# Kernel tuning notes

Measured on AMD Instinct MI355X. Metric: run time of the kernel, lower is better.

## Reference

```python
import jax, jax.numpy as jnp
import numpy as np

N_NODES = 40000
N_EDGES = 640000
D_IN = 128
D_OUT = 128


def setup_inputs() -> dict:
    key = jax.random.key(0)
    k_feat, k_src, k_dst, k_ws, k_wn = jax.random.split(key, 5)
    feat = jax.random.normal(k_feat, (N_NODES, D_IN), dtype=jnp.float32)
    src = jax.random.randint(k_src, (N_EDGES,), 0, N_NODES, dtype=jnp.int32)
    dst = jax.random.randint(k_dst, (N_EDGES,), 0, N_NODES, dtype=jnp.int32)
    # Glorot-ish init for the two dense layers
    scale = 1.0 / np.sqrt(D_IN)
    W_self = jax.random.normal(k_ws, (D_IN, D_OUT), dtype=jnp.float32) * scale
    W_neigh = jax.random.normal(k_wn, (D_IN, D_OUT), dtype=jnp.float32) * scale
    b_self = jnp.zeros((D_OUT,), dtype=jnp.float32)
    b_neigh = jnp.zeros((D_OUT,), dtype=jnp.float32)
    return {"feat": feat, "src": src, "dst": dst,
            "W_self": W_self, "b_self": b_self,
            "W_neigh": W_neigh, "b_neigh": b_neigh}


def reference(feat, src, dst, W_self, b_self, W_neigh, b_neigh):
    # --- mean aggregation: copy_src('h','m') + mean('m','neigh') ---
    # Gather source features along edges, segment-sum into dst, divide by in-degree.
    msgs = feat[src]  # [E, D_in]
    neigh_sum = jax.ops.segment_sum(msgs, dst, num_segments=N_NODES)  # [N, D_in]
    deg = jax.ops.segment_sum(jnp.ones((src.shape[0],), feat.dtype), dst,
                              num_segments=N_NODES)  # [N]
    # DGL mean reducer yields 0 for nodes with no incoming edges.
    h_neigh = neigh_sum / jnp.maximum(deg, 1.0)[:, None]
    # --- fc_self(h_self) + fc_neigh(h_neigh) ---
    rst = (feat @ W_self + b_self) + (h_neigh @ W_neigh + b_neigh)
    return rst
```

## Files before the change

kernel.cpp:

```cpp
#include <hip/hip_runtime.h>
#include <cstddef>

constexpr int NN  = 40000;
constexpr int NE  = 640000;
constexpr int DIM = 128;
constexpr int CAP = 48;
constexpr int PLANE = NN * 64;

typedef __attribute__((ext_vector_type(8))) short short8;
typedef __attribute__((ext_vector_type(4))) float floatx4;

__device__ __forceinline__ unsigned short f2bf(float x) {
    union { float f; unsigned int i; } v; v.f = x;
    unsigned int u = v.i;
    return (unsigned short)((u + 0x7fffu + ((u >> 16) & 1u)) >> 16);
}
__device__ __forceinline__ float bflo2f(unsigned int u) {
    union { unsigned int i; float f; } v; v.i = u << 16; return v.f;
}
__device__ __forceinline__ float bfhi2f(unsigned int u) {
    union { unsigned int i; float f; } v; v.i = u & 0xffff0000u; return v.f;
}

__global__ __launch_bounds__(256) void k_prep(
    const float* __restrict__ feat, const float* __restrict__ Wself,
    const float* __restrict__ Wneigh, unsigned short* __restrict__ featb,
    unsigned short* __restrict__ Wc, int* __restrict__ cnt)
{
    int b = blockIdx.x, t = threadIdx.x;
    if (b < 2500) {
        int idx8 = b * 256 + t;
        int n  = idx8 >> 4;
        int d0 = (idx8 & 15) << 3;
        const float4* fp =
            reinterpret_cast<const float4*>(feat + (size_t)n * DIM + d0);
        float4 v0 = fp[0], v1 = fp[1];
        unsigned int p0 = (unsigned int)f2bf(v0.x) | ((unsigned int)f2bf(v0.y) << 16);
        unsigned int p1 = (unsigned int)f2bf(v0.z) | ((unsigned int)f2bf(v0.w) << 16);
        unsigned int p2 = (unsigned int)f2bf(v1.x) | ((unsigned int)f2bf(v1.y) << 16);
        unsigned int p3 = (unsigned int)f2bf(v1.z) | ((unsigned int)f2bf(v1.w) << 16);
        int plane = d0 >> 6, off = d0 & 63;
        *reinterpret_cast<uint4*>(
            featb + (size_t)plane * PLANE + (size_t)n * 64 + off) =
            make_uint4(p0, p1, p2, p3);
    } else if (b < 2628) {
        int idx = (b - 2500) * 256 + t;
        int c = idx >> 13, n = (idx >> 6) & 127, kp = idx & 63;
        int k = c * 64 + kp;
        float w = (k < DIM) ? Wself[(size_t)k * DIM + n]
                            : Wneigh[(size_t)(k - DIM) * DIM + n];
        Wc[idx] = f2bf(w);
    } else {
        int i = (b - 2628) * 256 + t;
        if (i < NN) cnt[i] = 0;
    }
}

__global__ __launch_bounds__(256) void k_fill(
    const int* __restrict__ src, const int* __restrict__ dst,
    int* __restrict__ cnt, unsigned short* __restrict__ colf)
{
    int e = blockIdx.x * blockDim.x + threadIdx.x;
    if (e < NE) {
        int d = dst[e];
        int pos = atomicAdd(&cnt[d], 1);
        if (pos < CAP) colf[d * CAP + pos] = (unsigned short)src[e];
    }
}

__global__ __launch_bounds__(256) void k_gather(
    const unsigned int* __restrict__ fb32,
    const int* __restrict__ cnt,
    const unsigned short* __restrict__ colf,
    unsigned int* __restrict__ hnb32)
{
    int gtid = blockIdx.x * blockDim.x + threadIdx.x;
    int n = gtid >> 6;
    if (n >= NN) return;
    int lane = threadIdx.x & 63;

    int deg = cnt[n];
    int m = min(deg, CAP);
    int sv = (lane < m) ? (int)colf[n * CAP + lane] : 0;

    int vb = (lane >> 5) * (NN * 32) + (lane & 31);
    float ax0 = 0.f, ay0 = 0.f, ax1 = 0.f, ay1 = 0.f;
    int i = 0;
    for (; i + 3 < m; i += 4) {
        int s0 = __shfl(sv, i),     s1 = __shfl(sv, i + 1);
        int s2 = __shfl(sv, i + 2), s3 = __shfl(sv, i + 3);
        unsigned int u0 = fb32[vb + s0 * 32];
        unsigned int u1 = fb32[vb + s1 * 32];
        unsigned int u2 = fb32[vb + s2 * 32];
        unsigned int u3 = fb32[vb + s3 * 32];
        ax0 += bflo2f(u0); ay0 += bfhi2f(u0);
        ax1 += bflo2f(u1); ay1 += bfhi2f(u1);
        ax0 += bflo2f(u2); ay0 += bfhi2f(u2);
        ax1 += bflo2f(u3); ay1 += bfhi2f(u3);
    }
    for (; i < m; ++i) {
        int s0 = __shfl(sv, i);
        unsigned int u0 = fb32[vb + s0 * 32];
        ax0 += bflo2f(u0); ay0 += bfhi2f(u0);
    }
    float inv = 1.0f / fmaxf((float)deg, 1.0f);
    float ax = (ax0 + ax1) * inv, ay = (ay0 + ay1) * inv;
    hnb32[vb + n * 32] = (unsigned int)f2bf(ax) | ((unsigned int)f2bf(ay) << 16);
}

__global__ __launch_bounds__(320) void k_gemm(
    const unsigned short* __restrict__ featb,
    const unsigned short* __restrict__ hnb,
    const unsigned short* __restrict__ Wc,
    const float* __restrict__ bself, const float* __restrict__ bneigh,
    float* __restrict__ out)
{
    __shared__ unsigned short As[160 * 64];
    __shared__ unsigned short Bs[128 * 64];

    int t = threadIdx.x;
    int w = t >> 6;
    int lane = t & 63;
    int base_m = blockIdx.x * 160;

    floatx4 acc[2][8];
    #pragma unroll
    for (int a = 0; a < 2; ++a)
        #pragma unroll
        for (int b = 0; b < 8; ++b) acc[a][b] = (floatx4)0.f;

    for (int c = 0; c < 4; ++c) {
        const unsigned short* srcp =
            ((c < 2) ? featb + (size_t)c * PLANE
                     : hnb + (size_t)(c - 2) * PLANE) + (size_t)base_m * 64;
        #pragma unroll
        for (int it = 0; it < 4; ++it) {
            int slot = t + it * 320;
            __builtin_amdgcn_global_load_lds(
                (const __attribute__((address_space(1))) unsigned int*)(srcp + slot * 8),
                (__attribute__((address_space(3))) unsigned int*)(As + slot * 8),
                16, 0, 0);
        }
        if (t < 256) {
            const unsigned short* bp = Wc + (size_t)c * 128 * 64;
            #pragma unroll
            for (int it = 0; it < 4; ++it) {
                int slot = t + it * 256;
                __builtin_amdgcn_global_load_lds(
                    (const __attribute__((address_space(1))) unsigned int*)(bp + slot * 8),
                    (__attribute__((address_space(3))) unsigned int*)(Bs + slot * 8),
                    16, 0, 0);
            }
        }
        __syncthreads();

        #pragma unroll
        for (int s = 0; s < 2; ++s) {
            int koff = s * 32 + (lane >> 4) * 8;
            short8 af[2];
            #pragma unroll
            for (int mt = 0; mt < 2; ++mt) {
                int m = w * 32 + mt * 16 + (lane & 15);
                af[mt] = *reinterpret_cast<const short8*>(As + m * 64 + koff);
            }
            #pragma unroll
            for (int nt = 0; nt < 8; ++nt) {
                int n = nt * 16 + (lane & 15);
                short8 bf = *reinterpret_cast<const short8*>(Bs + n * 64 + koff);
                acc[0][nt] = __builtin_amdgcn_mfma_f32_16x16x32_bf16(
                    af[0], bf, acc[0][nt], 0, 0, 0);
                acc[1][nt] = __builtin_amdgcn_mfma_f32_16x16x32_bf16(
                    af[1], bf, acc[1][nt], 0, 0, 0);
            }
        }
        __syncthreads();
    }

    int colb = lane & 15;
    int quad = lane >> 4;
    #pragma unroll
    for (int nt = 0; nt < 8; ++nt) {
        int col = nt * 16 + colb;
        float bb = bself[col] + bneigh[col];
        #pragma unroll
        for (int mt = 0; mt < 2; ++mt) {
            #pragma unroll
            for (int r = 0; r < 4; ++r) {
                int row = base_m + w * 32 + mt * 16 + quad * 4 + r;
                out[(size_t)row * DIM + col] = acc[mt][nt][r] + bb;
            }
        }
    }
}

extern "C" void kernel_launch(void* const* d_in, const int* in_sizes, int n_in,
                              void* d_out, int out_size, void* d_ws, size_t ws_size,
                              hipStream_t stream)
{
    const float* feat   = (const float*)d_in[0];
    const int*   src    = (const int*)d_in[1];
    const int*   dst    = (const int*)d_in[2];
    const float* Wself  = (const float*)d_in[3];
    const float* bself  = (const float*)d_in[4];
    const float* Wneigh = (const float*)d_in[5];
    const float* bneigh = (const float*)d_in[6];
    float* out = (float*)d_out;

    char* ws = (char*)d_ws;
    unsigned short* featb = (unsigned short*)(ws);
    unsigned short* hnb   = (unsigned short*)(ws + 10240000);
    unsigned short* colf  = (unsigned short*)(ws + 20480000);
    unsigned short* Wc    = (unsigned short*)(ws + 24320000);
    int*            cnt   = (int*)(ws + 24385536);

    k_prep<<<2785, 256, 0, stream>>>(feat, Wself, Wneigh, featb, Wc, cnt);

    k_fill<<<(NE + 255) / 256, 256, 0, stream>>>(src, dst, cnt, colf);

    k_gather<<<(NN * 64) / 256, 256, 0, stream>>>(
        (const unsigned int*)featb, cnt, colf, (unsigned int*)hnb);

    k_gemm<<<NN / 160, 320, 0, stream>>>(featb, hnb, Wc, bself, bneigh, out);
}
```

Before: 148.7 us.

## Fuse neighbor gather into GEMM kernel, writing mean aggregates directly to LDS

New measurement: 210.0 us. +41.2%, slower.

```diff
diff --git a/kernel.cpp b/kernel.cpp
--- a/kernel.cpp
+++ b/kernel.cpp
@@ -68,49 +68,11 @@
     }
 }
 
-__global__ __launch_bounds__(256) void k_gather(
+__global__ __launch_bounds__(320) void k_gg(
+    const unsigned short* __restrict__ featb,
     const unsigned int* __restrict__ fb32,
     const int* __restrict__ cnt,
     const unsigned short* __restrict__ colf,
-    unsigned int* __restrict__ hnb32)
-{
-    int gtid = blockIdx.x * blockDim.x + threadIdx.x;
-    int n = gtid >> 6;
-    if (n >= NN) return;
-    int lane = threadIdx.x & 63;
-
-    int deg = cnt[n];
-    int m = min(deg, CAP);
-    int sv = (lane < m) ? (int)colf[n * CAP + lane] : 0;
-
-    int vb = (lane >> 5) * (NN * 32) + (lane & 31);
-    float ax0 = 0.f, ay0 = 0.f, ax1 = 0.f, ay1 = 0.f;
-    int i = 0;
-    for (; i + 3 < m; i += 4) {
-        int s0 = __shfl(sv, i),     s1 = __shfl(sv, i + 1);
-        int s2 = __shfl(sv, i + 2), s3 = __shfl(sv, i + 3);
-        unsigned int u0 = fb32[vb + s0 * 32];
-        unsigned int u1 = fb32[vb + s1 * 32];
-        unsigned int u2 = fb32[vb + s2 * 32];
-        unsigned int u3 = fb32[vb + s3 * 32];
-        ax0 += bflo2f(u0); ay0 += bfhi2f(u0);
-        ax1 += bflo2f(u1); ay1 += bfhi2f(u1);
-        ax0 += bflo2f(u2); ay0 += bfhi2f(u2);
-        ax1 += bflo2f(u3); ay1 += bfhi2f(u3);
-    }
-    for (; i < m; ++i) {
-        int s0 = __shfl(sv, i);
-        unsigned int u0 = fb32[vb + s0 * 32];
-        ax0 += bflo2f(u0); ay0 += bfhi2f(u0);
-    }
-    float inv = 1.0f / fmaxf((float)deg, 1.0f);
-    float ax = (ax0 + ax1) * inv, ay = (ay0 + ay1) * inv;
-    hnb32[vb + n * 32] = (unsigned int)f2bf(ax) | ((unsigned int)f2bf(ay) << 16);
-}
-
-__global__ __launch_bounds__(320) void k_gemm(
-    const unsigned short* __restrict__ featb,
-    const unsigned short* __restrict__ hnb,
     const unsigned short* __restrict__ Wc,
     const float* __restrict__ bself, const float* __restrict__ bneigh,
     float* __restrict__ out)
@@ -129,18 +91,11 @@
         #pragma unroll
         for (int b = 0; b < 8; ++b) acc[a][b] = (floatx4)0.f;
 
+    unsigned int* As32 = reinterpret_cast<unsigned int*>(As);
+    int j = lane >> 5;
+    int u = lane & 31;
+
     for (int c = 0; c < 4; ++c) {
-        const unsigned short* srcp =
-            ((c < 2) ? featb + (size_t)c * PLANE
-                     : hnb + (size_t)(c - 2) * PLANE) + (size_t)base_m * 64;
-        #pragma unroll
-        for (int it = 0; it < 4; ++it) {
-            int slot = t + it * 320;
-            __builtin_amdgcn_global_load_lds(
-                (const __attribute__((address_space(1))) unsigned int*)(srcp + slot * 8),
-                (__attribute__((address_space(3))) unsigned int*)(As + slot * 8),
-                16, 0, 0);
-        }
         if (t < 256) {
             const unsigned short* bp = Wc + (size_t)c * 128 * 64;
             #pragma unroll
@@ -150,6 +105,82 @@
                     (const __attribute__((address_space(1))) unsigned int*)(bp + slot * 8),
                     (__attribute__((address_space(3))) unsigned int*)(Bs + slot * 8),
                     16, 0, 0);
+            }
+        }
+
+        if (c < 2) {
+            const unsigned short* srcp =
+                featb + (size_t)c * PLANE + (size_t)base_m * 64;
+            #pragma unroll
+            for (int it = 0; it < 4; ++it) {
+                int slot = t + it * 320;
+                __builtin_amdgcn_global_load_lds(
+                    (const __attribute__((address_space(1))) unsigned int*)(srcp + slot * 8),
+                    (__attribute__((address_space(3))) unsigned int*)(As + slot * 8),
+                    16, 0, 0);
+            }
+        } else {
+            const unsigned int* pb = fb32 + (size_t)(c - 2) * (NN * 32);
+            for (int kk = 0; kk < 32; kk += 2) {
+                int ln0 = w * 32 + kk, ln1 = ln0 + 1;
+                int n0 = base_m + ln0, n1 = base_m + ln1;
+                int deg0 = cnt[n0], deg1 = cnt[n1];
+                int m0 = min(deg0, CAP), m1 = min(deg1, CAP);
+                int sv0 = (lane < m0) ? (int)colf[n0 * CAP + lane] : 0;
+                int sv1 = (lane < m1) ? (int)colf[n1 * CAP + lane] : 0;
+                float ax0 = 0.f, ay0 = 0.f, ax1 = 0.f, ay1 = 0.f;
+                {
+                    unsigned int va[8], vb_[8];
+                    int ia[8], ib[8];
+                    #pragma unroll
+                    for (int q = 0; q < 8; ++q) {
+                        ia[q] = 2 * q + j;
+                        ib[q] = 2 * q + j;
+                        int sa = __shfl(sv0, ia[q]);
+                        int sb = __shfl(sv1, ib[q]);
+                        va[q]  = pb[sa * 32 + u];
+                        vb_[q] = pb[sb * 32 + u];
+                    }
+                    #pragma unroll
+                    for (int q = 0; q < 8; ++q) {
+                        if (ia[q] < m0) { ax0 += bflo2f(va[q]);  ay0 += bfhi2f(va[q]); }
+                        if (ib[q] < m1) { ax1 += bflo2f(vb_[q]); ay1 += bfhi2f(vb_[q]); }
+                    }
+                }
+                for (int i = 16; i < m0; i += 16) {
+                    unsigned int va[8]; int ia[8];
+                    #pragma unroll
+                    for (int q = 0; q < 8; ++q) {
+                        ia[q] = i + 2 * q + j;
+                        int sa = __shfl(sv0, ia[q] < CAP ? ia[q] : 0);
+                        va[q] = pb[sa * 32 + u];
+                    }
+                    #pragma unroll
+                    for (int q = 0; q < 8; ++q)
+                        if (ia[q] < m0) { ax0 += bflo2f(va[q]); ay0 += bfhi2f(va[q]); }
+                }
+                for (int i = 16; i < m1; i += 16) {
+                    unsigned int vb2[8]; int ib[8];
+                    #pragma unroll
+                    for (int q = 0; q < 8; ++q) {
+                        ib[q] = i + 2 * q + j;
+                        int sb = __shfl(sv1, ib[q] < CAP ? ib[q] : 0);
+                        vb2[q] = pb[sb * 32 + u];
+                    }
+                    #pragma unroll
+                    for (int q = 0; q < 8; ++q)
+                        if (ib[q] < m1) { ax1 += bflo2f(vb2[q]); ay1 += bfhi2f(vb2[q]); }
+                }
+                ax0 += __shfl_xor(ax0, 32); ay0 += __shfl_xor(ay0, 32);
+                ax1 += __shfl_xor(ax1, 32); ay1 += __shfl_xor(ay1, 32);
+                if (lane < 32) {
+                    float inv0 = 1.0f / fmaxf((float)deg0, 1.0f);
+                    float inv1 = 1.0f / fmaxf((float)deg1, 1.0f);
+                    As32[ln0 * 32 + u] = (unsigned int)f2bf(ax0 * inv0)
+                                       | ((unsigned int)f2bf(ay0 * inv0) << 16);
+                    As32[ln1 * 32 + u] = (unsigned int)f2bf(ax1 * inv1)
+                                       | ((unsigned int)f2bf(ay1 * inv1) << 16);
+                }
             }
         }
         __syncthreads();
@@ -208,17 +239,14 @@
 
     char* ws = (char*)d_ws;
     unsigned short* featb = (unsigned short*)(ws);
-    unsigned short* hnb   = (unsigned short*)(ws + 10240000);
-    unsigned short* colf  = (unsigned short*)(ws + 20480000);
-    unsigned short* Wc    = (unsigned short*)(ws + 24320000);
-    int*            cnt   = (int*)(ws + 24385536);
+    unsigned short* colf  = (unsigned short*)(ws + 10240000);
+    unsigned short* Wc    = (unsigned short*)(ws + 14080000);
+    int*            cnt   = (int*)(ws + 14145536);
 
     k_prep<<<2785, 256, 0, stream>>>(feat, Wself, Wneigh, featb, Wc, cnt);
 
     k_fill<<<(NE + 255) / 256, 256, 0, stream>>>(src, dst, cnt, colf);
 
-    k_gather<<<(NN * 64) / 256, 256, 0, stream>>>(
-        (const unsigned int*)featb, cnt, colf, (unsigned int*)hnb);
-
-    k_gemm<<<NN / 160, 320, 0, stream>>>(featb, hnb, Wc, bself, bneigh, out);
-}
+    k_gg<<<NN / 160, 320, 0, stream>>>(
+        featb, (const unsigned int*)featb, cnt, colf, Wc, bself, bneigh, out);
+}
```

## Split gather into quarter-column planes and XOR-swizzle GEMM LDS tiles

Applied to the files above, without the earlier changes.

Result: slower. 165.8 us (+11.5%).

```diff
diff --git a/kernel.cpp b/kernel.cpp
--- a/kernel.cpp
+++ b/kernel.cpp
@@ -6,6 +6,7 @@
 constexpr int DIM = 128;
 constexpr int CAP = 48;
 constexpr int PLANE = NN * 64;
+constexpr int PL4   = NN * 32;
 
 typedef __attribute__((ext_vector_type(8))) short short8;
 typedef __attribute__((ext_vector_type(4))) float floatx4;
@@ -24,8 +25,9 @@
 
 __global__ __launch_bounds__(256) void k_prep(
     const float* __restrict__ feat, const float* __restrict__ Wself,
-    const float* __restrict__ Wneigh, unsigned short* __restrict__ featb,
-    unsigned short* __restrict__ Wc, int* __restrict__ cnt)
+    const float* __restrict__ Wneigh, unsigned short* __restrict__ featb2,
+    unsigned short* __restrict__ featb4, unsigned short* __restrict__ Wc,
+    int* __restrict__ cnt)
 {
     int b = blockIdx.x, t = threadIdx.x;
     if (b < 2500) {
@@ -39,10 +41,11 @@
         unsigned int p1 = (unsigned int)f2bf(v0.z) | ((unsigned int)f2bf(v0.w) << 16);
         unsigned int p2 = (unsigned int)f2bf(v1.x) | ((unsigned int)f2bf(v1.y) << 16);
         unsigned int p3 = (unsigned int)f2bf(v1.z) | ((unsigned int)f2bf(v1.w) << 16);
-        int plane = d0 >> 6, off = d0 & 63;
+        uint4 pk = make_uint4(p0, p1, p2, p3);
         *reinterpret_cast<uint4*>(
-            featb + (size_t)plane * PLANE + (size_t)n * 64 + off) =
-            make_uint4(p0, p1, p2, p3);
+            featb2 + (size_t)(d0 >> 6) * PLANE + (size_t)n * 64 + (d0 & 63)) = pk;
+        *reinterpret_cast<uint4*>(
+            featb4 + (size_t)(d0 >> 5) * PL4 + (size_t)n * 32 + (d0 & 31)) = pk;
     } else if (b < 2628) {
         int idx = (b - 2500) * 256 + t;
         int c = idx >> 13, n = (idx >> 6) & 127, kp = idx & 63;
@@ -69,43 +72,47 @@
 }
 
 __global__ __launch_bounds__(256) void k_gather(
-    const unsigned int* __restrict__ fb32,
+    const unsigned int* __restrict__ fb4,
     const int* __restrict__ cnt,
     const unsigned short* __restrict__ colf,
     unsigned int* __restrict__ hnb32)
 {
-    int gtid = blockIdx.x * blockDim.x + threadIdx.x;
-    int n = gtid >> 6;
-    if (n >= NN) return;
+    int b = blockIdx.x;
+    int c = b & 3;
+    int n = ((b >> 2) << 2) + (threadIdx.x >> 6);
     int lane = threadIdx.x & 63;
+    int j = lane >> 4;
+    int u = lane & 15;
 
     int deg = cnt[n];
     int m = min(deg, CAP);
     int sv = (lane < m) ? (int)colf[n * CAP + lane] : 0;
 
-    int vb = (lane >> 5) * (NN * 32) + (lane & 31);
-    float ax0 = 0.f, ay0 = 0.f, ax1 = 0.f, ay1 = 0.f;
-    int i = 0;
-    for (; i + 3 < m; i += 4) {
-        int s0 = __shfl(sv, i),     s1 = __shfl(sv, i + 1);
-        int s2 = __shfl(sv, i + 2), s3 = __shfl(sv, i + 3);
-        unsigned int u0 = fb32[vb + s0 * 32];
-        unsigned int u1 = fb32[vb + s1 * 32];
-        unsigned int u2 = fb32[vb + s2 * 32];
-        unsigned int u3 = fb32[vb + s3 * 32];
-        ax0 += bflo2f(u0); ay0 += bfhi2f(u0);
-        ax1 += bflo2f(u1); ay1 += bfhi2f(u1);
-        ax0 += bflo2f(u2); ay0 += bfhi2f(u2);
-        ax1 += bflo2f(u3); ay1 += bfhi2f(u3);
-    }
-    for (; i < m; ++i) {
-        int s0 = __shfl(sv, i);
-        unsigned int u0 = fb32[vb + s0 * 32];
-        ax0 += bflo2f(u0); ay0 += bfhi2f(u0);
-    }
-    float inv = 1.0f / fmaxf((float)deg, 1.0f);
-    float ax = (ax0 + ax1) * inv, ay = (ay0 + ay1) * inv;
-    hnb32[vb + n * 32] = (unsigned int)f2bf(ax) | ((unsigned int)f2bf(ay) << 16);
+    const unsigned int* pb = fb4 + (size_t)c * (NN * 16);
+    float ax = 0.f, ay = 0.f;
+    for (int i = 0; i < m; i += 16) {
+        int i0 = i + j, i1 = i + 4 + j, i2 = i + 8 + j, i3 = i + 12 + j;
+        int s0 = __shfl(sv, i0), s1 = __shfl(sv, i1);
+        int s2 = __shfl(sv, i2), s3 = __shfl(sv, i3);
+        unsigned int v0 = pb[s0 * 16 + u];
+        unsigned int v1 = pb[s1 * 16 + u];
+        unsigned int v2 = pb[s2 * 16 + u];
+        unsigned int v3 = pb[s3 * 16 + u];
+        if (i0 < m) { ax += bflo2f(v0); ay += bfhi2f(v0); }
+        if (i1 < m) { ax += bflo2f(v1); ay += bfhi2f(v1); }
+        if (i2 < m) { ax += bflo2f(v2); ay += bfhi2f(v2); }
+        if (i3 < m) { ax += bflo2f(v3); ay += bfhi2f(v3); }
+    }
+    ax += __shfl_xor(ax, 16); ay += __shfl_xor(ay, 16);
+    ax += __shfl_xor(ax, 32); ay += __shfl_xor(ay, 32);
+    if (lane < 16) {
+        float inv = 1.0f / fmaxf((float)deg, 1.0f);
+        unsigned int pk = (unsigned int)f2bf(ax * inv)
+                        | ((unsigned int)f2bf(ay * inv) << 16);
+        __builtin_nontemporal_store(
+            pk, hnb32 + (size_t)(c >> 1) * (NN * 32)
+                      + (size_t)n * 32 + (c & 1) * 16 + u);
+    }
 }
 
 __global__ __launch_bounds__(320) void k_gemm(
@@ -135,38 +142,44 @@
                      : hnb + (size_t)(c - 2) * PLANE) + (size_t)base_m * 64;
         #pragma unroll
         for (int it = 0; it < 4; ++it) {
-            int slot = t + it * 320;
+            int s = t + it * 320;
+            int m = s >> 3, g = s & 7;
+            const unsigned short* sa = srcp + m * 64 + ((g ^ (m & 7)) << 3);
             __builtin_amdgcn_global_load_lds(
-                (const __attribute__((address_space(1))) unsigned int*)(srcp + slot * 8),
-                (__attribute__((address_space(3))) unsigned int*)(As + slot * 8),
+                (const __attribute__((address_space(1))) unsigned int*)sa,
+                (__attribute__((address_space(3))) unsigned int*)(As + s * 8),
                 16, 0, 0);
         }
         if (t < 256) {
             const unsigned short* bp = Wc + (size_t)c * 128 * 64;
             #pragma unroll
             for (int it = 0; it < 4; ++it) {
-                int slot = t + it * 256;
+                int s = t + it * 256;
+                int n = s >> 3, g = s & 7;
+                const unsigned short* sb = bp + n * 64 + ((g ^ (n & 7)) << 3);
                 __builtin_amdgcn_global_load_lds(
-                    (const __attribute__((address_space(1))) unsigned int*)(bp + slot * 8),
-                    (__attribute__((address_space(3))) unsigned int*)(Bs + slot * 8),
+                    (const __attribute__((address_space(1))) unsigned int*)sb,
+                    (__attribute__((address_space(3))) unsigned int*)(Bs + s * 8),
                     16, 0, 0);
             }
         }
         __syncthreads();
 
         #pragma unroll
-        for (int s = 0; s < 2; ++s) {
-            int koff = s * 32 + (lane >> 4) * 8;
+        for (int sstep = 0; sstep < 2; ++sstep) {
+            int gk = sstep * 4 + (lane >> 4);
             short8 af[2];
             #pragma unroll
             for (int mt = 0; mt < 2; ++mt) {
                 int m = w * 32 + mt * 16 + (lane & 15);
-                af[mt] = *reinterpret_cast<const short8*>(As + m * 64 + koff);
+                af[mt] = *reinterpret_cast<const short8*>(
+                    As + m * 64 + ((gk ^ (m & 7)) << 3));
             }
             #pragma unroll
             for (int nt = 0; nt < 8; ++nt) {
                 int n = nt * 16 + (lane & 15);
-                short8 bf = *reinterpret_cast<const short8*>(Bs + n * 64 + koff);
+                short8 bf = *reinterpret_cast<const short8*>(
+                    Bs + n * 64 + ((gk ^ (n & 7)) << 3));
                 acc[0][nt] = __builtin_amdgcn_mfma_f32_16x16x32_bf16(
                     af[0], bf, acc[0][nt], 0, 0, 0);
                 acc[1][nt] = __builtin_amdgcn_mfma_f32_16x16x32_bf16(
@@ -207,18 +220,20 @@
     float* out = (float*)d_out;
 
     char* ws = (char*)d_ws;
-    unsigned short* featb = (unsigned short*)(ws);
-    unsigned short* hnb   = (unsigned short*)(ws + 10240000);
-    unsigned short* colf  = (unsigned short*)(ws + 20480000);
-    unsigned short* Wc    = (unsigned short*)(ws + 24320000);
-    int*            cnt   = (int*)(ws + 24385536);
-
-    k_prep<<<2785, 256, 0, stream>>>(feat, Wself, Wneigh, featb, Wc, cnt);
+    unsigned short* featb2 = (unsigned short*)(ws);
+    unsigned short* hnb    = (unsigned short*)(ws + 10240000);
+    unsigned short* colf   = (unsigned short*)(ws + 20480000);
+    unsigned short* Wc     = (unsigned short*)(ws + 24320000);
+    int*            cnt    = (int*)(ws + 24385536);
+    unsigned short* featb4 = (unsigned short*)(ws + 24545536);
+
+    k_prep<<<2785, 256, 0, stream>>>(feat, Wself, Wneigh,
+                                     featb2, featb4, Wc, cnt);
 
     k_fill<<<(NE + 255) / 256, 256, 0, stream>>>(src, dst, cnt, colf);
 
-    k_gather<<<(NN * 64) / 256, 256, 0, stream>>>(
-        (const unsigned int*)featb, cnt, colf, (unsigned int*)hnb);
-
-    k_gemm<<<NN / 160, 320, 0, stream>>>(featb, hnb, Wc, bself, bneigh, out);
-}
+    k_gather<<<NN, 256, 0, stream>>>(
+        (const unsigned int*)featb4, cnt, colf, (unsigned int*)hnb);
+
+    k_gemm<<<NN / 160, 320, 0, stream>>>(featb2, hnb, Wc, bself, bneigh, out);
+}
```

## Vectorize gather with 16-byte loads across lane groups and swizzle GEMM LDS

Applied to the files above, without the earlier changes.

Result: faster. 145.1 us (-2.4%).

```diff
diff --git a/kernel.cpp b/kernel.cpp
--- a/kernel.cpp
+++ b/kernel.cpp
@@ -69,43 +69,78 @@
 }
 
 __global__ __launch_bounds__(256) void k_gather(
-    const unsigned int* __restrict__ fb32,
+    const uint4* __restrict__ fb,
     const int* __restrict__ cnt,
     const unsigned short* __restrict__ colf,
-    unsigned int* __restrict__ hnb32)
+    uint4* __restrict__ hnb4)
 {
     int gtid = blockIdx.x * blockDim.x + threadIdx.x;
     int n = gtid >> 6;
     if (n >= NN) return;
     int lane = threadIdx.x & 63;
+    int g = lane >> 4;
+    int j = lane & 15;
 
     int deg = cnt[n];
     int m = min(deg, CAP);
     int sv = (lane < m) ? (int)colf[n * CAP + lane] : 0;
 
-    int vb = (lane >> 5) * (NN * 32) + (lane & 31);
-    float ax0 = 0.f, ay0 = 0.f, ax1 = 0.f, ay1 = 0.f;
-    int i = 0;
-    for (; i + 3 < m; i += 4) {
-        int s0 = __shfl(sv, i),     s1 = __shfl(sv, i + 1);
-        int s2 = __shfl(sv, i + 2), s3 = __shfl(sv, i + 3);
-        unsigned int u0 = fb32[vb + s0 * 32];
-        unsigned int u1 = fb32[vb + s1 * 32];
-        unsigned int u2 = fb32[vb + s2 * 32];
-        unsigned int u3 = fb32[vb + s3 * 32];
-        ax0 += bflo2f(u0); ay0 += bfhi2f(u0);
-        ax1 += bflo2f(u1); ay1 += bfhi2f(u1);
-        ax0 += bflo2f(u2); ay0 += bfhi2f(u2);
-        ax1 += bflo2f(u3); ay1 += bfhi2f(u3);
-    }
-    for (; i < m; ++i) {
-        int s0 = __shfl(sv, i);
-        unsigned int u0 = fb32[vb + s0 * 32];
-        ax0 += bflo2f(u0); ay0 += bfhi2f(u0);
-    }
-    float inv = 1.0f / fmaxf((float)deg, 1.0f);
-    float ax = (ax0 + ax1) * inv, ay = (ay0 + ay1) * inv;
-    hnb32[vb + n * 32] = (unsigned int)f2bf(ax) | ((unsigned int)f2bf(ay) << 16);
+    size_t rb = (size_t)(j >> 3) * (NN * 8) + (j & 7);
+    float a0 = 0.f, a1 = 0.f, a2 = 0.f, a3 = 0.f;
+    float a4 = 0.f, a5 = 0.f, a6 = 0.f, a7 = 0.f;
+
+    for (int i = 0; i < m; i += 16) {
+        int i0 = i + g, i1 = i + 4 + g, i2 = i + 8 + g, i3 = i + 12 + g;
+        int s0 = __shfl(sv, i0), s1 = __shfl(sv, i1);
+        int s2 = __shfl(sv, i2), s3 = __shfl(sv, i3);
+        uint4 v0 = fb[rb + (size_t)s0 * 8];
+        uint4 v1 = fb[rb + (size_t)s1 * 8];
+        uint4 v2 = fb[rb + (size_t)s2 * 8];
+        uint4 v3 = fb[rb + (size_t)s3 * 8];
+        unsigned int z0 = (i0 < m) ? 0xffffffffu : 0u;
+        unsigned int z1 = (i1 < m) ? 0xffffffffu : 0u;
+        unsigned int z2 = (i2 < m) ? 0xffffffffu : 0u;
+        unsigned int z3 = (i3 < m) ? 0xffffffffu : 0u;
+        v0.x &= z0; v0.y &= z0; v0.z &= z0; v0.w &= z0;
+        v1.x &= z1; v1.y &= z1; v1.z &= z1; v1.w &= z1;
+        v2.x &= z2; v2.y &= z2; v2.z &= z2; v2.w &= z2;
+        v3.x &= z3; v3.y &= z3; v3.z &= z3; v3.w &= z3;
+        a0 += bflo2f(v0.x); a1 += bfhi2f(v0.x);
+        a2 += bflo2f(v0.y); a3 += bfhi2f(v0.y);
+        a4 += bflo2f(v0.z); a5 += bfhi2f(v0.z);
+        a6 += bflo2f(v0.w); a7 += bfhi2f(v0.w);
+        a0 += bflo2f(v1.x); a1 += bfhi2f(v1.x);
+        a2 += bflo2f(v1.y); a3 += bfhi2f(v1.y);
+        a4 += bflo2f(v1.z); a5 += bfhi2f(v1.z);
+        a6 += bflo2f(v1.w); a7 += bfhi2f(v1.w);
+        a0 += bflo2f(v2.x); a1 += bfhi2f(v2.x);
+        a2 += bflo2f(v2.y); a3 += bfhi2f(v2.y);
+        a4 += bflo2f(v2.z); a5 += bfhi2f(v2.z);
+        a6 += bflo2f(v2.w); a7 += bfhi2f(v2.w);
+        a0 += bflo2f(v3.x); a1 += bfhi2f(v3.x);
+        a2 += bflo2f(v3.y); a3 += bfhi2f(v3.y);
+        a4 += bflo2f(v3.z); a5 += bfhi2f(v3.z);
+        a6 += bflo2f(v3.w); a7 += bfhi2f(v3.w);
+    }
+
+    a0 += __shfl_xor(a0, 16); a1 += __shfl_xor(a1, 16);
+    a2 += __shfl_xor(a2, 16); a3 += __shfl_xor(a3, 16);
+    a4 += __shfl_xor(a4, 16); a5 += __shfl_xor(a5, 16);
+    a6 += __shfl_xor(a6, 16); a7 += __shfl_xor(a7, 16);
+    a0 += __shfl_xor(a0, 32); a1 += __shfl_xor(a1, 32);
+    a2 += __shfl_xor(a2, 32); a3 += __shfl_xor(a3, 32);
+    a4 += __shfl_xor(a4, 32); a5 += __shfl_xor(a5, 32);
+    a6 += __shfl_xor(a6, 32); a7 += __shfl_xor(a7, 32);
+
+    if (lane < 16) {
+        float inv = 1.0f / fmaxf((float)deg, 1.0f);
+        uint4 pk;
+        pk.x = (unsigned int)f2bf(a0 * inv) | ((unsigned int)f2bf(a1 * inv) << 16);
+        pk.y = (unsigned int)f2bf(a2 * inv) | ((unsigned int)f2bf(a3 * inv) << 16);
+        pk.z = (unsigned int)f2bf(a4 * inv) | ((unsigned int)f2bf(a5 * inv) << 16);
+        pk.w = (unsigned int)f2bf(a6 * inv) | ((unsigned int)f2bf(a7 * inv) << 16);
+        hnb4[rb + (size_t)n * 8] = pk;
+    }
 }
 
 __global__ __launch_bounds__(320) void k_gemm(
@@ -135,38 +170,44 @@
                      : hnb + (size_t)(c - 2) * PLANE) + (size_t)base_m * 64;
         #pragma unroll
         for (int it = 0; it < 4; ++it) {
-            int slot = t + it * 320;
+            int s = t + it * 320;
+            int m = s >> 3, g = s & 7;
+            const unsigned short* sa = srcp + m * 64 + ((g ^ (m & 7)) << 3);
             __builtin_amdgcn_global_load_lds(
-                (const __attribute__((address_space(1))) unsigned int*)(srcp + slot * 8),
-                (__attribute__((address_space(3))) unsigned int*)(As + slot * 8),
+                (const __attribute__((address_space(1))) unsigned int*)sa,
+                (__attribute__((address_space(3))) unsigned int*)(As + s * 8),
                 16, 0, 0);
         }
         if (t < 256) {
             const unsigned short* bp = Wc + (size_t)c * 128 * 64;
             #pragma unroll
             for (int it = 0; it < 4; ++it) {
-                int slot = t + it * 256;
+                int s = t + it * 256;
+                int n = s >> 3, g = s & 7;
+                const unsigned short* sb = bp + n * 64 + ((g ^ (n & 7)) << 3);
                 __builtin_amdgcn_global_load_lds(
-                    (const __attribute__((address_space(1))) unsigned int*)(bp + slot * 8),
-                    (__attribute__((address_space(3))) unsigned int*)(Bs + slot * 8),
+                    (const __attribute__((address_space(1))) unsigned int*)sb,
+                    (__attribute__((address_space(3))) unsigned int*)(Bs + s * 8),
                     16, 0, 0);
             }
         }
         __syncthreads();
 
         #pragma unroll
-        for (int s = 0; s < 2; ++s) {
-            int koff = s * 32 + (lane >> 4) * 8;
+        for (int sstep = 0; sstep < 2; ++sstep) {
+            int gk = sstep * 4 + (lane >> 4);
             short8 af[2];
             #pragma unroll
             for (int mt = 0; mt < 2; ++mt) {
                 int m = w * 32 + mt * 16 + (lane & 15);
-                af[mt] = *reinterpret_cast<const short8*>(As + m * 64 + koff);
+                af[mt] = *reinterpret_cast<const short8*>(
+                    As + m * 64 + ((gk ^ (m & 7)) << 3));
             }
             #pragma unroll
             for (int nt = 0; nt < 8; ++nt) {
                 int n = nt * 16 + (lane & 15);
-                short8 bf = *reinterpret_cast<const short8*>(Bs + n * 64 + koff);
+                short8 bf = *reinterpret_cast<const short8*>(
+                    Bs + n * 64 + ((gk ^ (n & 7)) << 3));
                 acc[0][nt] = __builtin_amdgcn_mfma_f32_16x16x32_bf16(
                     af[0], bf, acc[0][nt], 0, 0, 0);
                 acc[1][nt] = __builtin_amdgcn_mfma_f32_16x16x32_bf16(
@@ -218,7 +259,7 @@
     k_fill<<<(NE + 255) / 256, 256, 0, stream>>>(src, dst, cnt, colf);
 
     k_gather<<<(NN * 64) / 256, 256, 0, stream>>>(
-        (const unsigned int*)featb, cnt, colf, (unsigned int*)hnb);
+        (const uint4*)featb, cnt, colf, (uint4*)hnb);
 
     k_gemm<<<NN / 160, 320, 0, stream>>>(featb, hnb, Wc, bself, bneigh, out);
 }
```
